# Optimization experiments

Measured on AMD Instinct MI355X. Metric: run time of the kernel, lower is better.

Reference implementation:

```python
import jax, jax.numpy as jnp
import numpy as np

N_HEADS = 4

def layernorm(x, g, b):
    m = jnp.mean(x, -1, keepdims=True)
    v = jnp.var(x, -1, keepdims=True)
    return (x - m) / jnp.sqrt(v + 1e-5) * g + b

def conv1d(x, w, b, pad):
    y = jax.lax.conv_general_dilated(x, w, (1,), [(pad, pad)], dimension_numbers=('NCH', 'OIH', 'NCH'))
    return y + b[None, :, None]

def bn_eval(x, g, b, m, v):
    return (x - m[None, :, None]) / jnp.sqrt(v[None, :, None] + 1e-5) * g[None, :, None] + b[None, :, None]

def maxpool(x, k):
    return jax.lax.reduce_window(x, -jnp.inf, jax.lax.max, (1, 1, k), (1, 1, k), 'VALID')

def _forward(x, conv1_w, conv1_b, bn1_g, bn1_b, bn1_m, bn1_v, conv2_w, conv2_b, bn2_g, bn2_b, bn2_m, bn2_v, adj_prior, log_weights, gat_n1_g, gat_n1_b, gat_qkv_w, gat_qkv_b, gat_out_w, gat_out_b, gat_n2_g, gat_n2_b, gat_f1_w, gat_f1_b, gat_f2_w, gat_f2_b, gatn_g, gatn_b, gru_wih, gru_whh, gru_bih, gru_bhh, gate_w, gate_b):
    B, C, T = x.shape
    D = conv2_w.shape[0]
    dk = D // N_HEADS
    scale = dk ** -0.5
    # --- per-channel temporal CNN: (B,C,T) -> (B,C,T',D), T' = T//16 ---
    h = x.reshape(B * C, 1, T)
    h = maxpool(jax.nn.gelu(bn_eval(conv1d(h, conv1_w, conv1_b, 3), bn1_g, bn1_b, bn1_m, bn1_v), approximate=False), 4)
    h = maxpool(jax.nn.gelu(bn_eval(conv1d(h, conv2_w, conv2_b, 2), bn2_g, bn2_b, bn2_m, bn2_v), approximate=False), 4)
    Tp = h.shape[-1]
    h = jnp.transpose(h, (0, 2, 1)).reshape(B, C, Tp, D)
    # --- spectral dynamic adjacency ---
    h_avg = h.mean(axis=2)                                   # (B,C,D)
    hc = h_avg - h_avg.mean(-1, keepdims=True)
    hn = hc / (jnp.linalg.norm(hc, axis=-1, keepdims=True) + 1e-8)
    feat_corr = jnp.einsum('bcd,bed->bce', hn, hn)
    Xp = jnp.abs(jnp.fft.rfft(x, axis=-1))
    Xn = Xp / (jnp.linalg.norm(Xp, axis=-1, keepdims=True) + 1e-8)
    spec_coh = jnp.einsum('bcf,bef->bce', Xn, Xn)
    prior = (adj_prior + adj_prior.T)[None]
    w = jax.nn.softmax(log_weights)
    adj = w[0] * feat_corr + w[1] * spec_coh + w[2] * prior  # (B,C,C)
    # --- GAT stack over the C-node channel graph at every timestep ---
    ht = jnp.transpose(h, (0, 2, 1, 3)).reshape(B * Tp, C, D)
    adj_t = jnp.broadcast_to(adj[:, None], (B, Tp, C, C)).reshape(B * Tp, C, C)
    L = gat_qkv_w.shape[0]
    for l in range(L):
        hn1 = layernorm(ht, gat_n1_g[l], gat_n1_b[l])
        qkv = (hn1 @ gat_qkv_w[l].T + gat_qkv_b[l]).reshape(B * Tp, C, 3, N_HEADS, dk)
        q = jnp.moveaxis(qkv[:, :, 0], 1, 2)                 # (N,H,C,dk)
        k = jnp.moveaxis(qkv[:, :, 1], 1, 2)
        v = jnp.moveaxis(qkv[:, :, 2], 1, 2)
        attn = jnp.einsum('nhqd,nhkd->nhqk', q, k) * scale + adj_t[:, None]
        attn = jax.nn.softmax(attn, axis=-1)                 # dropout off (eval)
        out = jnp.einsum('nhqk,nhkd->nhqd', attn, v)
        out = jnp.moveaxis(out, 1, 2).reshape(B * Tp, C, D)
        ht = ht + out @ gat_out_w[l].T + gat_out_b[l]
        hn2 = layernorm(ht, gat_n2_g[l], gat_n2_b[l])
        ffn = jax.nn.gelu(hn2 @ gat_f1_w[l].T + gat_f1_b[l], approximate=False) @ gat_f2_w[l].T + gat_f2_b[l]
        ht = ht + ffn
    ht = layernorm(ht, gatn_g, gatn_b)
    hs = ht.reshape(B, Tp, C, D).transpose(0, 2, 1, 3).reshape(B * C, Tp, D)
    # --- bidirectional GRU (1 layer), final hidden states only ---
    G = gru_whh.shape[-1]
    def gru_last(xs, wih, whh, bih, bhh):
        def step(hprev, xt):
            gi = xt @ wih.T + bih
            gh = hprev @ whh.T + bhh
            ir, iz, inn = jnp.split(gi, 3, -1)
            hr, hz, hnn = jnp.split(gh, 3, -1)
            r = jax.nn.sigmoid(ir + hr)
            z = jax.nn.sigmoid(iz + hz)
            n = jnp.tanh(inn + r * hnn)
            hnew = (1.0 - z) * n + z * hprev
            return hnew, None
        h0 = jnp.zeros((xs.shape[0], G), xs.dtype)
        hl, _ = jax.lax.scan(step, h0, jnp.moveaxis(xs, 1, 0))
        return hl
    h_f = gru_last(hs, gru_wih[0], gru_whh[0], gru_bih[0], gru_bhh[0])
    h_b = gru_last(hs[:, ::-1], gru_wih[1], gru_whh[1], gru_bih[1], gru_bhh[1])
    h_out = jnp.concatenate([h_f, h_b], -1).reshape(B, C, 2 * G)
    # --- channel-attention readout ---
    gate = jax.nn.sigmoid(h_out @ gate_w.T + gate_b)         # (B,C,1)
    readout = (h_out * gate).sum(1) / (gate.sum(1) + 1e-8)   # (B,2G)
    return readout, adj, gate

def setup_inputs() -> dict:
    key = jax.random.key(0)
    ks = iter(jax.random.split(key, 64))
    B, C, T = 32, 16, 4096
    D, L, G = 64, 2, 64
    def rn(shape, s=0.08):
        return jax.random.normal(next(ks), shape, jnp.float32) * s
    return dict(
        x=jax.random.normal(next(ks), (B, C, T), jnp.float32),
        conv1_w=rn((32, 1, 7), 0.2), conv1_b=rn((32,)),
        bn1_g=jnp.ones((32,)), bn1_b=jnp.zeros((32,)), bn1_m=jnp.zeros((32,)), bn1_v=jnp.ones((32,)),
        conv2_w=rn((D, 32, 5), 0.1), conv2_b=rn((D,)),
        bn2_g=jnp.ones((D,)), bn2_b=jnp.zeros((D,)), bn2_m=jnp.zeros((D,)), bn2_v=jnp.ones((D,)),
        adj_prior=rn((C, C), 0.1), log_weights=jnp.zeros((3,)),
        gat_n1_g=jnp.ones((L, D)), gat_n1_b=jnp.zeros((L, D)),
        gat_qkv_w=rn((L, 3 * D, D)), gat_qkv_b=jnp.zeros((L, 3 * D)),
        gat_out_w=rn((L, D, D)), gat_out_b=jnp.zeros((L, D)),
        gat_n2_g=jnp.ones((L, D)), gat_n2_b=jnp.zeros((L, D)),
        gat_f1_w=rn((L, 2 * D, D)), gat_f1_b=jnp.zeros((L, 2 * D)),
        gat_f2_w=rn((L, D, 2 * D)), gat_f2_b=jnp.zeros((L, D)),
        gatn_g=jnp.ones((D,)), gatn_b=jnp.zeros((D,)),
        gru_wih=rn((2, 3 * G, D)), gru_whh=rn((2, 3 * G, G)),
        gru_bih=jnp.zeros((2, 3 * G)), gru_bhh=jnp.zeros((2, 3 * G)),
        gate_w=rn((1, 2 * G)), gate_b=jnp.zeros((1,)),
    )

def reference(x, conv1_w, conv1_b, bn1_g, bn1_b, bn1_m, bn1_v, conv2_w, conv2_b, bn2_g, bn2_b, bn2_m, bn2_v, adj_prior, log_weights, gat_n1_g, gat_n1_b, gat_qkv_w, gat_qkv_b, gat_out_w, gat_out_b, gat_n2_g, gat_n2_b, gat_f1_w, gat_f1_b, gat_f2_w, gat_f2_b, gatn_g, gatn_b, gru_wih, gru_whh, gru_bih, gru_bhh, gate_w, gate_b):
    return _forward(x, conv1_w, conv1_b, bn1_g, bn1_b, bn1_m, bn1_v, conv2_w, conv2_b, bn2_g, bn2_b, bn2_m, bn2_v, adj_prior, log_weights, gat_n1_g, gat_n1_b, gat_qkv_w, gat_qkv_b, gat_out_w, gat_out_b, gat_n2_g, gat_n2_b, gat_f1_w, gat_f1_b, gat_f2_w, gat_f2_b, gatn_g, gatn_b, gru_wih, gru_whh, gru_bih, gru_bhh, gate_w, gate_b)
```

## Files before the change

### kernel.cpp

```cpp
#include <hip/hip_runtime.h>
#include <hip/hip_bf16.h>
#include <math.h>

typedef __hip_bfloat16 bf16;
typedef unsigned short ushort_t;
typedef __attribute__((ext_vector_type(8))) short short8;
typedef __attribute__((ext_vector_type(4))) float f32x4;

__device__ __forceinline__ float b2f(bf16 v) { return __bfloat162float(v); }
__device__ __forceinline__ bf16 f2b(float v) { return __float2bfloat16(v); }
__device__ __forceinline__ float bflo(unsigned u) { return __uint_as_float(u << 16); }
__device__ __forceinline__ float bfhi(unsigned u) { return __uint_as_float(u & 0xffff0000u); }
__device__ __forceinline__ float sigmoidf_(float x) { return 1.0f / (1.0f + __expf(-x)); }

__device__ __forceinline__ float geluf(float x) {
    float z = x * 0.70710678118654752f;
    float az = fabsf(z);
    float t = 1.0f / (1.0f + 0.3275911f * az);
    float poly = ((((1.061405429f * t - 1.453152027f) * t + 1.421413741f) * t
                   - 0.284496736f) * t + 0.254829592f) * t;
    float erfa = 1.0f - poly * __expf(-z * z);
    float er = (z < 0.f) ? -erfa : erfa;
    return 0.5f * x * (1.0f + er);
}

__device__ __forceinline__ unsigned pack2bf(float a, float b) {
    unsigned ua = __float_as_uint(a); ua = (ua + 0x7FFFu + ((ua >> 16) & 1u)) >> 16;
    unsigned ub = __float_as_uint(b); ub = (ub + 0x7FFFu + ((ub >> 16) & 1u)) >> 16;
    return ua | (ub << 16);
}
__device__ __forceinline__ ushort_t f2bu(float v) {
    unsigned u = __float_as_uint(v);
    u = (u + 0x7FFFu + ((u >> 16) & 1u)) >> 16;
    return (ushort_t)u;
}

__global__ __launch_bounds__(256) void k_detect(const unsigned* __restrict__ x, int* __restrict__ flag)
{
    __shared__ int cnt;
    if (threadIdx.x == 0) cnt = 0;
    __syncthreads();
    unsigned u = x[threadIdx.x] & 0xFFFFu;
    float f = __uint_as_float(u << 16);
    float a = fabsf(f);
    int sane = (f == 0.0f) || (a > 1e-8f && a < 1e4f);
    atomicAdd(&cnt, sane);
    __syncthreads();
    if (threadIdx.x == 0) *flag = (cnt >= 160) ? 1 : 0;
}

struct InPtrs { const void* p[35]; };
struct InOffs { int off[35]; int sz[35]; };

__global__ __launch_bounds__(256) void k_convert(InPtrs P, InOffs O, int total,
                                                 const int* __restrict__ flag,
                                                 float* __restrict__ cvt)
{
    int idx = blockIdx.x * 256 + threadIdx.x;
    if (idx >= total) return;
    int isb = *flag;
    float v = 0.f;
#pragma unroll 1
    for (int s = 0; s < 35; s++) {
        int rel = idx - O.off[s];
        if (rel >= 0 && rel < O.sz[s]) {
            v = isb ? b2f(((const bf16*)P.p[s])[rel]) : ((const float*)P.p[s])[rel];
            break;
        }
    }
    cvt[idx] = v;
}

__global__ __launch_bounds__(256) void k_pack(const float* __restrict__ qw, const float* __restrict__ ow,
                                              const float* __restrict__ f1w, const float* __restrict__ f2w,
                                              const float* __restrict__ gwih, const float* __restrict__ gwhh,
                                              const float* __restrict__ c2w,
                                              unsigned* __restrict__ dst)
{
    int i = blockIdx.x * 256 + threadIdx.x;
    if (i >= 62464) return;
    if (i >= 57344) {
        int j0 = (i - 57344) * 2;
        int tap = j0 >> 11, rem = j0 & 2047;
        int d = rem >> 5, ic = rem & 31;
        dst[i] = pack2bf(c2w[d * 160 + ic * 5 + tap], c2w[d * 160 + (ic + 1) * 5 + tap]);
        return;
    }
    const float* s; int rel;
    if (i < 12288)      { s = qw;   rel = i; }
    else if (i < 16384) { s = ow;   rel = i - 12288; }
    else if (i < 24576) { s = f1w;  rel = i - 16384; }
    else if (i < 32768) { s = f2w;  rel = i - 24576; }
    else if (i < 45056) { s = gwih; rel = i - 32768; }
    else                { s = gwhh; rel = i - 45056; }
    dst[i] = pack2bf(s[2 * rel], s[2 * rel + 1]);
}

__global__ __launch_bounds__(256) void k_cnn(
    const float* __restrict__ x, const float* __restrict__ c1w, const float* __restrict__ c1b,
    const float* __restrict__ bn1g, const float* __restrict__ bn1b, const float* __restrict__ bn1m, const float* __restrict__ bn1v,
    const float* __restrict__ c2b,
    const float* __restrict__ bn2g, const float* __restrict__ bn2b, const float* __restrict__ bn2m, const float* __restrict__ bn2v,
    const ushort_t* __restrict__ w2pk,
    float* __restrict__ h_main)
{
    __shared__ float ubuf[4352];
    __shared__ ushort_t h1t[260 * 40];
    __shared__ float A2s[64], B2s[64];
    int bc = blockIdx.x, t = threadIdx.x;
    int l = t & 63, w = t >> 6;
    int lo = l & 15, quad = l >> 4;

    if (t < 64) {
        float s = bn2g[t] * rsqrtf(bn2v[t] + 1e-5f);
        A2s[t] = s; B2s[t] = (c2b[t] - bn2m[t]) * s + bn2b[t];
    }
    int icp = t & 15;
    float w1r[2][7], A1r[2], B1r[2];
#pragma unroll
    for (int s = 0; s < 2; s++) {
        int ic = icp * 2 + s;
#pragma unroll
        for (int k = 0; k < 7; k++) w1r[s][k] = c1w[ic * 7 + k];
        float sc = bn1g[ic] * rsqrtf(bn1v[ic] + 1e-5f);
        A1r[s] = sc; B1r[s] = (c1b[ic] - bn1m[ic]) * sc + bn1b[ic];
    }
    short8 Afr[4][5];
#pragma unroll
    for (int dt = 0; dt < 4; dt++)
#pragma unroll
        for (int tap = 0; tap < 5; tap++)
            Afr[dt][tap] = *(const short8*)(w2pk + ((tap * 64 + dt * 16 + lo) * 32 + quad * 8));

    const float* xrow = x + (size_t)bc * 4096;
    for (int tile = 0; tile < 4; tile++) {
        int X0 = 1024 * tile - 11;
        for (int i = t; i < 1056; i += 256) {
            int g = X0 + i;
            ubuf[i] = (g >= 0 && g < 4096) ? xrow[g] : 0.0f;
        }
        __syncthreads();
        for (int pos = (t >> 4); pos < 260; pos += 16) {
            const float4* xw = (const float4*)&ubuf[4 * pos];
            float4 fa = xw[0], fb = xw[1], fc = xw[2];
            float xv[12] = {fa.x, fa.y, fa.z, fa.w, fb.x, fb.y, fb.z, fb.w,
                            fc.x, fc.y, fc.z, fc.w};
            int t1pg = tile * 256 + pos - 2;
            bool ok = (t1pg >= 0 && t1pg < 1024);
            float res[2];
#pragma unroll
            for (int s = 0; s < 2; s++) {
                float a0 = 0.f, a1 = 0.f, a2 = 0.f, a3 = 0.f;
#pragma unroll
                for (int k = 0; k < 7; k++) {
                    float wv = w1r[s][k];
                    a0 += xv[k] * wv;     a1 += xv[k + 1] * wv;
                    a2 += xv[k + 2] * wv; a3 += xv[k + 3] * wv;
                }
                float A = A1r[s], B = B1r[s];
                a0 = a0 * A + B; a1 = a1 * A + B; a2 = a2 * A + B; a3 = a3 * A + B;
                float mx = fmaxf(fmaxf(a0, a1), fmaxf(a2, a3));
                float mn = fminf(fminf(a0, a1), fminf(a2, a3));
                res[s] = ok ? fmaxf(geluf(mx), geluf(mn)) : 0.0f;
            }
            ((unsigned*)h1t)[pos * 20 + icp] = pack2bf(res[0], res[1]);
        }
        __syncthreads();
        float* houtile = ubuf;
#pragma unroll
        for (int ni = 0; ni < 4; ni++) {
            int nt = w * 4 + ni;
            short8 bf[5];
#pragma unroll
            for (int tap = 0; tap < 5; tap++)
                bf[tap] = *(const short8*)&h1t[(nt * 16 + lo + tap) * 40 + quad * 8];
#pragma unroll
            for (int dt = 0; dt < 4; dt++) {
                f32x4 acc = {0.f, 0.f, 0.f, 0.f};
#pragma unroll
                for (int tap = 0; tap < 5; tap++)
                    acc = __builtin_amdgcn_mfma_f32_16x16x32_bf16(Afr[dt][tap], bf[tap], acc, 0, 0, 0);
                const float4 a2 = *(const float4*)&A2s[dt * 16 + quad * 4];
                const float4 b2 = *(const float4*)&B2s[dt * 16 + quad * 4];
                float a2a[4] = {a2.x, a2.y, a2.z, a2.w};
                float b2a[4] = {b2.x, b2.y, b2.z, b2.w};
#pragma unroll
                for (int r = 0; r < 4; r++) {
                    float v = acc[r] * a2a[r] + b2a[r];
                    float o1 = __shfl_xor(v, 1);
                    float mx = fmaxf(v, o1), mn = fminf(v, o1);
                    float mx2 = __shfl_xor(mx, 2), mn2 = __shfl_xor(mn, 2);
                    mx = fmaxf(mx, mx2); mn = fminf(mn, mn2);
                    float res = fmaxf(geluf(mx), geluf(mn));
                    if ((lo & 3) == 0)
                        houtile[(nt * 4 + (lo >> 2)) * 68 + dt * 16 + quad * 4 + r] = res;
                }
            }
        }
        __syncthreads();
        float* dst = h_main + (size_t)bc * 16384 + tile * 4096;
        for (int i = t * 4; i < 4096; i += 1024) {
            float4 v = *(const float4*)&ubuf[(i >> 6) * 68 + (i & 63)];
            *(float4*)&dst[i] = v;
        }
        __syncthreads();
    }
}

__global__ __launch_bounds__(512) void k_fft(const float* __restrict__ x, float* __restrict__ Xn)
{
    __shared__ float re[4096];
    __shared__ float im[4096];
    __shared__ float red[8];
    int bc = blockIdx.x, t = threadIdx.x;
    const float* xr = x + (size_t)bc * 4096;
    for (int i = t; i < 4096; i += 512) {
        int r = __brev((unsigned)i) >> 20;
        re[r] = xr[i];
        im[r] = 0.f;
    }
    __syncthreads();
    for (int s = 1; s <= 12; s++) {
        int half = 1 << (s - 1);
        float ang = -6.283185307179586f / (float)(1 << s);
        for (int m = t; m < 2048; m += 512) {
            int j = m & (half - 1);
            int pos = ((m >> (s - 1)) << s) | j;
            float sn, cs;
            __sincosf(ang * (float)j, &sn, &cs);
            float ur = re[pos], ui = im[pos];
            float vr = re[pos + half], vi = im[pos + half];
            float tr = vr * cs - vi * sn;
            float ti = vr * sn + vi * cs;
            re[pos] = ur + tr; im[pos] = ui + ti;
            re[pos + half] = ur - tr; im[pos + half] = ui - ti;
        }
        __syncthreads();
    }
    float mag[5];
    float ss = 0.f;
    int cnt = 0;
    for (int f = t; f <= 2048; f += 512) {
        float m2 = re[f] * re[f] + im[f] * im[f];
        mag[cnt++] = sqrtf(m2);
        ss += m2;
    }
    for (int off = 32; off; off >>= 1) ss += __shfl_xor(ss, off, 64);
    if ((t & 63) == 0) red[t >> 6] = ss;
    __syncthreads();
    float tot = 0.f;
#pragma unroll
    for (int i = 0; i < 8; i++) tot += red[i];
    float inv = 1.0f / (sqrtf(tot) + 1e-8f);
    cnt = 0;
    for (int f = t; f <= 2048; f += 512) Xn[(size_t)bc * 2049 + f] = mag[cnt++] * inv;
}

__global__ __launch_bounds__(64) void k_havg(const float* __restrict__ hm, float* __restrict__ hnf)
{
    int bc = blockIdx.x, d = threadIdx.x;
    const float* base = hm + (size_t)bc * 16384;
    float s = 0.f;
    for (int tp = 0; tp < 256; tp++) s += base[tp * 64 + d];
    float avg = s * (1.0f / 256.0f);
    float tot = avg;
    for (int off = 32; off; off >>= 1) tot += __shfl_xor(tot, off, 64);
    float hc = avg - tot * (1.0f / 64.0f);
    float sq = hc * hc;
    for (int off = 32; off; off >>= 1) sq += __shfl_xor(sq, off, 64);
    hnf[bc * 64 + d] = hc / (sqrtf(sq) + 1e-8f);
}

__global__ __launch_bounds__(256) void k_adj(
    const float* __restrict__ Xn, const float* __restrict__ hnf,
    const float* __restrict__ prior, const float* __restrict__ logw,
    float* __restrict__ adjw, void* __restrict__ out, const int* __restrict__ flag)
{
    __shared__ float xt[16][257];
    __shared__ float hh[16 * 64];
    int b = blockIdx.x, t = threadIdx.x;
    int c = t >> 4, e = t & 15;
    for (int i = t; i < 1024; i += 256) hh[i] = hnf[b * 1024 + i];
    __syncthreads();
    float fc = 0.f;
    for (int d = 0; d < 64; d++) fc += hh[c * 64 + d] * hh[e * 64 + d];
    float sc = 0.f;
    const float* Xb = Xn + (size_t)b * 16 * 2049;
    for (int f0 = 0; f0 < 2048; f0 += 256) {
        __syncthreads();
        for (int i = t; i < 16 * 256; i += 256) {
            int rr = i >> 8, ff = i & 255;
            xt[rr][ff] = Xb[rr * 2049 + f0 + ff];
        }
        __syncthreads();
        for (int ff = 0; ff < 256; ff++) sc += xt[c][ff] * xt[e][ff];
    }
    sc += Xb[c * 2049 + 2048] * Xb[e * 2049 + 2048];
    float l0 = logw[0], l1 = logw[1], l2 = logw[2];
    float mx = fmaxf(l0, fmaxf(l1, l2));
    float e0 = __expf(l0 - mx), e1 = __expf(l1 - mx), e2 = __expf(l2 - mx);
    float isum = 1.0f / (e0 + e1 + e2);
    float pr = prior[c * 16 + e] + prior[e * 16 + c];
    float v = (e0 * fc + e1 * sc + e2 * pr) * isum;
    adjw[b * 256 + t] = v;
    if (*flag) ((bf16*)out)[4096 + b * 256 + t] = f2b(v);
    else       ((float*)out)[4096 + b * 256 + t] = v;
}

__device__ __forceinline__ void ln_wave(const float (*ht)[68], ushort_t (*out)[72],
                                        const float* __restrict__ g, const float* __restrict__ bp,
                                        int quad, int lo)
{
    float v[16];
    const float4* row = (const float4*)(&ht[lo][quad * 16]);
#pragma unroll
    for (int i = 0; i < 4; i++) {
        float4 a = row[i];
        v[4 * i] = a.x; v[4 * i + 1] = a.y; v[4 * i + 2] = a.z; v[4 * i + 3] = a.w;
    }
    float s = 0.f;
#pragma unroll
    for (int i = 0; i < 16; i++) s += v[i];
    s += __shfl_xor(s, 16); s += __shfl_xor(s, 32);
    float mean = s * (1.0f / 64.0f);
    float q = 0.f;
#pragma unroll
    for (int i = 0; i < 16; i++) { float d = v[i] - mean; q += d * d; }
    q += __shfl_xor(q, 16); q += __shfl_xor(q, 32);
    float rstd = rsqrtf(q * (1.0f / 64.0f) + 1e-5f);
    const float4* gp = (const float4*)(g + quad * 16);
    const float4* bb4 = (const float4*)(bp + quad * 16);
    unsigned* orow = (unsigned*)(&out[lo][quad * 16]);
#pragma unroll
    for (int i = 0; i < 4; i++) {
        float4 gg = gp[i], bb = bb4[i];
        float o0 = (v[4 * i] - mean) * rstd * gg.x + bb.x;
        float o1 = (v[4 * i + 1] - mean) * rstd * gg.y + bb.y;
        float o2 = (v[4 * i + 2] - mean) * rstd * gg.z + bb.z;
        float o3 = (v[4 * i + 3] - mean) * rstd * gg.w + bb.w;
        orow[2 * i] = pack2bf(o0, o1);
        orow[2 * i + 1] = pack2bf(o2, o3);
    }
}

__global__ __launch_bounds__(256) void k_gat(
    const float* __restrict__ hm, const float* __restrict__ adjw,
    const ushort_t* __restrict__ wpk,
    const float* __restrict__ qb_, const float* __restrict__ ob_,
    const float* __restrict__ f1b_, const float* __restrict__ f2b_,
    const float* __restrict__ n1g_, const float* __restrict__ n1b_,
    const float* __restrict__ n2g_, const float* __restrict__ n2b_,
    const float* __restrict__ gng, const float* __restrict__ gnb,
    ushort_t* __restrict__ hmb)
{
    __shared__ float htw_all[4][16][68];
    __shared__ ushort_t hnw_all[4][16][72];
    __shared__ ushort_t qkb_all[4][16][200];
    __shared__ ushort_t pb_all[4][16][72];
    __shared__ ushort_t vt_all[4][64][24];
    int t = threadIdx.x;
    int w = t >> 6, l = t & 63;
    int quad = l >> 4, lo = l & 15;
    int n = blockIdx.x * 4 + w;
    int b = n >> 8, tp = n & 255;
    float (*htw)[68] = htw_all[w];
    ushort_t (*hnw)[72] = hnw_all[w];
    ushort_t (*qkb)[200] = qkb_all[w];
    ushort_t (*pb)[72] = pb_all[w];
    ushort_t (*vt)[24] = vt_all[w];
    const float* src = hm + (size_t)b * 16 * 16384 + (size_t)tp * 64;
#pragma unroll
    for (int c = 0; c < 16; c++) htw[c][l] = src[(size_t)c * 16384 + l];
    float adjr[4];
#pragma unroll
    for (int r = 0; r < 4; r++) adjr[r] = adjw[b * 256 + (quad * 4 + r) * 16 + lo];

    for (int layer = 0; layer < 2; layer++) {
        const ushort_t* wq  = wpk + layer * 12288;
        const ushort_t* wo  = wpk + 24576 + layer * 4096;
        const ushort_t* wf1 = wpk + 32768 + layer * 8192;
        const ushort_t* wf2 = wpk + 49152 + layer * 8192;
        const float* qb = qb_ + layer * 192;
        const float* ob = ob_ + layer * 64;
        const float* f1b = f1b_ + layer * 128;
        const float* f2b = f2b_ + layer * 64;

        ln_wave(htw, hnw, n1g_ + layer * 64, n1b_ + layer * 64, quad, lo);

        short8 a0 = *(const short8*)&hnw[lo][quad * 8];
        short8 a1 = *(const short8*)&hnw[lo][32 + quad * 8];
#pragma unroll
        for (int nt = 0; nt < 12; nt++) {
            const ushort_t* wr = wq + (nt * 16 + lo) * 64 + quad * 8;
            short8 b0 = *(const short8*)wr;
            short8 b1 = *(const short8*)(wr + 32);
            f32x4 acc = {0.f, 0.f, 0.f, 0.f};
            acc = __builtin_amdgcn_mfma_f32_16x16x32_bf16(a0, b0, acc, 0, 0, 0);
            acc = __builtin_amdgcn_mfma_f32_16x16x32_bf16(a1, b1, acc, 0, 0, 0);
            float bias = qb[nt * 16 + lo];
            if (nt < 8) {
#pragma unroll
                for (int r = 0; r < 4; r++) qkb[quad * 4 + r][nt * 16 + lo] = f2bu(acc[r] + bias);
            } else {
#pragma unroll
                for (int r = 0; r < 4; r++) vt[(nt - 8) * 16 + lo][quad * 4 + r] = f2bu(acc[r] + bias);
            }
        }

        short8 zf = {0, 0, 0, 0, 0, 0, 0, 0};
#pragma unroll
        for (int h = 0; h < 4; h++) {
            short8 qf = zf, kf = zf;
            if (quad < 2) {
                qf = *(const short8*)&qkb[lo][h * 16 + quad * 8];
                kf = *(const short8*)&qkb[lo][64 + h * 16 + quad * 8];
            }
            f32x4 s4 = {0.f, 0.f, 0.f, 0.f};
            s4 = __builtin_amdgcn_mfma_f32_16x16x32_bf16(qf, kf, s4, 0, 0, 0);
#pragma unroll
            for (int r = 0; r < 4; r++) {
                float sv = s4[r] * 0.25f + adjr[r];
                float mx = sv;
                mx = fmaxf(mx, __shfl_xor(mx, 1));
                mx = fmaxf(mx, __shfl_xor(mx, 2));
                mx = fmaxf(mx, __shfl_xor(mx, 4));
                mx = fmaxf(mx, __shfl_xor(mx, 8));
                float e = __expf(sv - mx);
                float sm = e;
                sm += __shfl_xor(sm, 1);
                sm += __shfl_xor(sm, 2);
                sm += __shfl_xor(sm, 4);
                sm += __shfl_xor(sm, 8);
                pb[quad * 4 + r][h * 16 + lo] = f2bu(e / sm);
            }
        }
#pragma unroll
        for (int h = 0; h < 4; h++) {
            short8 pf = zf, vf = zf;
            if (quad < 2) {
                pf = *(const short8*)&pb[lo][h * 16 + quad * 8];
                vf = *(const short8*)&vt[h * 16 + lo][quad * 8];
            }
            f32x4 oc = {0.f, 0.f, 0.f, 0.f};
            oc = __builtin_amdgcn_mfma_f32_16x16x32_bf16(pf, vf, oc, 0, 0, 0);
#pragma unroll
            for (int r = 0; r < 4; r++) qkb[quad * 4 + r][h * 16 + lo] = f2bu(oc[r]);
        }
        short8 pa0 = *(const short8*)&qkb[lo][quad * 8];
        short8 pa1 = *(const short8*)&qkb[lo][32 + quad * 8];
#pragma unroll
        for (int nt = 0; nt < 4; nt++) {
            const ushort_t* wr = wo + (nt * 16 + lo) * 64 + quad * 8;
            short8 b0 = *(const short8*)wr;
            short8 b1 = *(const short8*)(wr + 32);
            f32x4 acc = {0.f, 0.f, 0.f, 0.f};
            acc = __builtin_amdgcn_mfma_f32_16x16x32_bf16(pa0, b0, acc, 0, 0, 0);
            acc = __builtin_amdgcn_mfma_f32_16x16x32_bf16(pa1, b1, acc, 0, 0, 0);
            float bias = ob[nt * 16 + lo];
#pragma unroll
            for (int r = 0; r < 4; r++) htw[quad * 4 + r][nt * 16 + lo] += acc[r] + bias;
        }
        ln_wave(htw, hnw, n2g_ + layer * 64, n2b_ + layer * 64, quad, lo);
        short8 fa0 = *(const short8*)&hnw[lo][quad * 8];
        short8 fa1 = *(const short8*)&hnw[lo][32 + quad * 8];
#pragma unroll
        for (int nt = 0; nt < 8; nt++) {
            const ushort_t* wr = wf1 + (nt * 16 + lo) * 64 + quad * 8;
            short8 b0 = *(const short8*)wr;
            short8 b1 = *(const short8*)(wr + 32);
            f32x4 acc = {0.f, 0.f, 0.f, 0.f};
            acc = __builtin_amdgcn_mfma_f32_16x16x32_bf16(fa0, b0, acc, 0, 0, 0);
            acc = __builtin_amdgcn_mfma_f32_16x16x32_bf16(fa1, b1, acc, 0, 0, 0);
            float bias = f1b[nt * 16 + lo];
#pragma unroll
            for (int r = 0; r < 4; r++) qkb[quad * 4 + r][nt * 16 + lo] = f2bu(geluf(acc[r] + bias));
        }
        short8 ga[4];
#pragma unroll
        for (int kb = 0; kb < 4; kb++) ga[kb] = *(const short8*)&qkb[lo][kb * 32 + quad * 8];
#pragma unroll
        for (int nt = 0; nt < 4; nt++) {
            const ushort_t* wr = wf2 + (nt * 16 + lo) * 128 + quad * 8;
            f32x4 acc = {0.f, 0.f, 0.f, 0.f};
#pragma unroll
            for (int kb = 0; kb < 4; kb++) {
                short8 bb = *(const short8*)(wr + kb * 32);
                acc = __builtin_amdgcn_mfma_f32_16x16x32_bf16(ga[kb], bb, acc, 0, 0, 0);
            }
            float bias = f2b[nt * 16 + lo];
#pragma unroll
            for (int r = 0; r < 4; r++) htw[quad * 4 + r][nt * 16 + lo] += acc[r] + bias;
        }
    }
    {
        float v[16];
        const float4* row = (const float4*)(&htw[lo][quad * 16]);
#pragma unroll
        for (int i = 0; i < 4; i++) {
            float4 a = row[i];
            v[4 * i] = a.x; v[4 * i + 1] = a.y; v[4 * i + 2] = a.z; v[4 * i + 3] = a.w;
        }
        float s = 0.f;
#pragma unroll
        for (int i = 0; i < 16; i++) s += v[i];
        s += __shfl_xor(s, 16); s += __shfl_xor(s, 32);
        float mean = s * (1.0f / 64.0f);
        float q = 0.f;
#pragma unroll
        for (int i = 0; i < 16; i++) { float d = v[i] - mean; q += d * d; }
        q += __shfl_xor(q, 16); q += __shfl_xor(q, 32);
        float rstd = rsqrtf(q * (1.0f / 64.0f) + 1e-5f);
        const float4* gp = (const float4*)(gng + quad * 16);
        const float4* bb4 = (const float4*)(gnb + quad * 16);
        unsigned u[8];
#pragma unroll
        for (int i = 0; i < 4; i++) {
            float4 gg = gp[i], bb = bb4[i];
            float o0 = (v[4 * i] - mean) * rstd * gg.x + bb.x;
            float o1 = (v[4 * i + 1] - mean) * rstd * gg.y + bb.y;
            float o2 = (v[4 * i + 2] - mean) * rstd * gg.z + bb.z;
            float o3 = (v[4 * i + 3] - mean) * rstd * gg.w + bb.w;
            u[2 * i] = pack2bf(o0, o1);
            u[2 * i + 1] = pack2bf(o2, o3);
        }
        ushort_t* dst = hmb + (size_t)(b * 16 + lo) * 16384 + (size_t)tp * 64 + quad * 16;
        ((uint4*)dst)[0] = make_uint4(u[0], u[1], u[2], u[3]);
        ((uint4*)dst)[1] = make_uint4(u[4], u[5], u[6], u[7]);
    }
}

__global__ __launch_bounds__(256) void k_gru(
    const ushort_t* __restrict__ hmb, const ushort_t* __restrict__ wgru,
    const float* __restrict__ bih_, const float* __restrict__ bhh_,
    float* __restrict__ h_out)
{
    __shared__ ushort_t hbuf[2][16][72];
    int t = threadIdx.x;
    int w = t >> 6, l = t & 63;
    int ln = l & 15, qd = l >> 4;
    int dir = blockIdx.x >> 5;
    int cseq0 = (blockIdx.x & 31) * 16;
    const ushort_t* wih = wgru + dir * 12288;
    const ushort_t* whh = wgru + 24576 + dir * 12288;
    const ushort_t* pr0 = wih + ((w)*16 + ln) * 64 + qd * 8;
    const ushort_t* pz0 = wih + ((4 + w)*16 + ln) * 64 + qd * 8;
    const ushort_t* pn0 = wih + ((8 + w)*16 + ln) * 64 + qd * 8;
    const ushort_t* hr0 = whh + ((w)*16 + ln) * 64 + qd * 8;
    const ushort_t* hz0 = whh + ((4 + w)*16 + ln) * 64 + qd * 8;
    const ushort_t* hn0 = whh + ((8 + w)*16 + ln) * 64 + qd * 8;
    short8 wi_r0 = *(const short8*)pr0, wi_r1 = *(const short8*)(pr0 + 32);
    short8 wi_z0 = *(const short8*)pz0, wi_z1 = *(const short8*)(pz0 + 32);
    short8 wi_n0 = *(const short8*)pn0, wi_n1 = *(const short8*)(pn0 + 32);
    short8 wh_r0 = *(const short8*)hr0, wh_r1 = *(const short8*)(hr0 + 32);
    short8 wh_z0 = *(const short8*)hz0, wh_z1 = *(const short8*)(hz0 + 32);
    short8 wh_n0 = *(const short8*)hn0, wh_n1 = *(const short8*)(hn0 + 32);
    int d = w * 16 + ln;
    float bs_r = bih_[dir * 192 + d] + bhh_[dir * 192 + d];
    float bs_z = bih_[dir * 192 + 64 + d] + bhh_[dir * 192 + 64 + d];
    float bi_n = bih_[dir * 192 + 128 + d];
    float bh_n = bhh_[dir * 192 + 128 + d];
    const ushort_t* xrow = hmb + (size_t)(cseq0 + ln) * 16384 + qd * 8;
    for (int i = t; i < 2 * 16 * 72; i += 256) ((ushort_t*)hbuf)[i] = 0;
    float h_old[4] = {0.f, 0.f, 0.f, 0.f};

    int s0 = dir ? 255 : 0;
    int s1 = dir ? 254 : 1;
    int s2 = dir ? 253 : 2;
    short8 xc0 = *(const short8*)(xrow + s0 * 64);
    short8 xc1 = *(const short8*)(xrow + s0 * 64 + 32);
    short8 xA0 = *(const short8*)(xrow + s1 * 64);
    short8 xA1 = *(const short8*)(xrow + s1 * 64 + 32);
    short8 xB0 = *(const short8*)(xrow + s2 * 64);
    short8 xB1 = *(const short8*)(xrow + s2 * 64 + 32);
    f32x4 axr = {0.f, 0.f, 0.f, 0.f}, axz = {0.f, 0.f, 0.f, 0.f}, axn = {0.f, 0.f, 0.f, 0.f};
    axr = __builtin_amdgcn_mfma_f32_16x16x32_bf16(xc0, wi_r0, axr, 0, 0, 0);
    axr = __builtin_amdgcn_mfma_f32_16x16x32_bf16(xc1, wi_r1, axr, 0, 0, 0);
    axz = __builtin_amdgcn_mfma_f32_16x16x32_bf16(xc0, wi_z0, axz, 0, 0, 0);
    axz = __builtin_amdgcn_mfma_f32_16x16x32_bf16(xc1, wi_z1, axz, 0, 0, 0);
    axn = __builtin_amdgcn_mfma_f32_16x16x32_bf16(xc0, wi_n0, axn, 0, 0, 0);
    axn = __builtin_amdgcn_mfma_f32_16x16x32_bf16(xc1, wi_n1, axn, 0, 0, 0);
    __syncthreads();
#pragma unroll 2
    for (int step = 0; step < 256; step++) {
        int cur = step & 1, nxt = cur ^ 1;
        f32x4 nxr = {0.f, 0.f, 0.f, 0.f}, nxz = {0.f, 0.f, 0.f, 0.f}, nxn = {0.f, 0.f, 0.f, 0.f};
        nxr = __builtin_amdgcn_mfma_f32_16x16x32_bf16(xA0, wi_r0, nxr, 0, 0, 0);
        nxr = __builtin_amdgcn_mfma_f32_16x16x32_bf16(xA1, wi_r1, nxr, 0, 0, 0);
        nxz = __builtin_amdgcn_mfma_f32_16x16x32_bf16(xA0, wi_z0, nxz, 0, 0, 0);
        nxz = __builtin_amdgcn_mfma_f32_16x16x32_bf16(xA1, wi_z1, nxz, 0, 0, 0);
        nxn = __builtin_amdgcn_mfma_f32_16x16x32_bf16(xA0, wi_n0, nxn, 0, 0, 0);
        nxn = __builtin_amdgcn_mfma_f32_16x16x32_bf16(xA1, wi_n1, nxn, 0, 0, 0);
        xA0 = xB0; xA1 = xB1;
        int tl = step + 3 > 255 ? 255 : step + 3;
        int sf = dir ? 255 - tl : tl;
        xB0 = *(const short8*)(xrow + sf * 64);
        xB1 = *(const short8*)(xrow + sf * 64 + 32);
        short8 ah0 = *(const short8*)&hbuf[cur][ln][qd * 8];
        short8 ah1 = *(const short8*)&hbuf[cur][ln][32 + qd * 8];
        f32x4 ar = axr, az = axz;
        f32x4 anh = {0.f, 0.f, 0.f, 0.f};
        ar = __builtin_amdgcn_mfma_f32_16x16x32_bf16(ah0, wh_r0, ar, 0, 0, 0);
        ar = __builtin_amdgcn_mfma_f32_16x16x32_bf16(ah1, wh_r1, ar, 0, 0, 0);
        az = __builtin_amdgcn_mfma_f32_16x16x32_bf16(ah0, wh_z0, az, 0, 0, 0);
        az = __builtin_amdgcn_mfma_f32_16x16x32_bf16(ah1, wh_z1, az, 0, 0, 0);
        anh = __builtin_amdgcn_mfma_f32_16x16x32_bf16(ah0, wh_n0, anh, 0, 0, 0);
        anh = __builtin_amdgcn_mfma_f32_16x16x32_bf16(ah1, wh_n1, anh, 0, 0, 0);
#pragma unroll
        for (int r = 0; r < 4; r++) {
            float gr = sigmoidf_(ar[r] + bs_r);
            float gz = sigmoidf_(az[r] + bs_z);
            float nin = (axn[r] + bi_n) + gr * (anh[r] + bh_n);
            nin = fminf(fmaxf(nin, -15.f), 15.f);
            float e = __expf(-2.f * nin);
            float gn = (1.f - e) / (1.f + e);
            float hn = gn + gz * (h_old[r] - gn);
            h_old[r] = hn;
            hbuf[nxt][qd * 4 + r][d] = f2bu(hn);
        }
        asm volatile("s_waitcnt lgkmcnt(0)\n\ts_barrier" ::: "memory");
        axr = nxr; axz = nxz; axn = nxn;
    }
#pragma unroll
    for (int r = 0; r < 4; r++)
        h_out[(size_t)(cseq0 + qd * 4 + r) * 128 + dir * 64 + d] = h_old[r];
}

__global__ __launch_bounds__(128) void k_readout(
    const float* __restrict__ h_out, const float* __restrict__ gw, const float* __restrict__ gb,
    void* __restrict__ out, const int* __restrict__ flag)
{
    __shared__ float gate_s[16];
    __shared__ float gws[128];
    int b = blockIdx.x, t = threadIdx.x;
    gws[t] = gw[t];
    __syncthreads();
    int isb = *flag;
    if (t < 16) {
        const float* hr = h_out + (size_t)(b * 16 + t) * 128;
        float acc = gb[0];
        for (int k = 0; k < 128; k++) acc += hr[k] * gws[k];
        float g = sigmoidf_(acc);
        gate_s[t] = g;
        if (isb) ((bf16*)out)[12288 + b * 16 + t] = f2b(g);
        else     ((float*)out)[12288 + b * 16 + t] = g;
    }
    __syncthreads();
    float den = 1e-8f;
#pragma unroll
    for (int c = 0; c < 16; c++) den += gate_s[c];
    float num = 0.f;
#pragma unroll
    for (int c = 0; c < 16; c++) num += h_out[(size_t)(b * 16 + c) * 128 + t] * gate_s[c];
    float v = num / den;
    if (isb) ((bf16*)out)[b * 128 + t] = f2b(v);
    else     ((float*)out)[b * 128 + t] = v;
}

extern "C" void kernel_launch(void* const* d_in, const int* in_sizes, int n_in,
                              void* d_out, int out_size, void* d_ws, size_t ws_size,
                              hipStream_t stream)
{
    int* flag = (int*)d_ws;
    float* cvt = (float*)((char*)d_ws + 256);

    InPtrs P;
    InOffs O;
    int cum = 0;
    for (int i = 0; i < 35; i++) {
        P.p[i] = d_in[i];
        O.off[i] = cum;
        O.sz[i] = in_sizes[i];
        cum += (in_sizes[i] + 7) & ~7;
    }
    int total = cum;

    const float* x     = cvt + O.off[0];
    const float* c1w   = cvt + O.off[1];
    const float* c1b   = cvt + O.off[2];
    const float* bn1g  = cvt + O.off[3];
    const float* bn1b  = cvt + O.off[4];
    const float* bn1m  = cvt + O.off[5];
    const float* bn1v  = cvt + O.off[6];
    const float* c2w   = cvt + O.off[7];
    const float* c2b   = cvt + O.off[8];
    const float* bn2g  = cvt + O.off[9];
    const float* bn2b  = cvt + O.off[10];
    const float* bn2m  = cvt + O.off[11];
    const float* bn2v  = cvt + O.off[12];
    const float* prior = cvt + O.off[13];
    const float* logw  = cvt + O.off[14];
    const float* n1g   = cvt + O.off[15];
    const float* n1b   = cvt + O.off[16];
    const float* qkvw  = cvt + O.off[17];
    const float* qkvb  = cvt + O.off[18];
    const float* outw  = cvt + O.off[19];
    const float* outb  = cvt + O.off[20];
    const float* n2g   = cvt + O.off[21];
    const float* n2b   = cvt + O.off[22];
    const float* f1w   = cvt + O.off[23];
    const float* f1b   = cvt + O.off[24];
    const float* f2w   = cvt + O.off[25];
    const float* f2b_  = cvt + O.off[26];
    const float* gng   = cvt + O.off[27];
    const float* gnb   = cvt + O.off[28];
    const float* gwih  = cvt + O.off[29];
    const float* gwhh  = cvt + O.off[30];
    const float* gbih  = cvt + O.off[31];
    const float* gbhh  = cvt + O.off[32];
    const float* gatew = cvt + O.off[33];
    const float* gateb = cvt + O.off[34];

    float* fbase = cvt + ((total + 63) & ~63);
    float* hm   = fbase;
    float* Xn   = hm + 8388608;
    float* hnf  = Xn + 1049088;
    float* adjw = hnf + 32768;
    float* hout = adjw + 8192;
    unsigned* wpk = (unsigned*)(hout + 65536);
    ushort_t* hmb = (ushort_t*)(wpk + 62464);

    k_detect<<<1, 256, 0, stream>>>((const unsigned*)d_in[0], flag);
    k_convert<<<(total + 255) / 256, 256, 0, stream>>>(P, O, total, flag, cvt);
    k_pack<<<244, 256, 0, stream>>>(qkvw, outw, f1w, f2w, gwih, gwhh, c2w, wpk);
    k_cnn<<<512, 256, 0, stream>>>(x, c1w, c1b, bn1g, bn1b, bn1m, bn1v,
                                   c2b, bn2g, bn2b, bn2m, bn2v,
                                   (const ushort_t*)(wpk + 57344), hm);
    k_fft<<<512, 512, 0, stream>>>(x, Xn);
    k_havg<<<512, 64, 0, stream>>>(hm, hnf);
    k_adj<<<32, 256, 0, stream>>>(Xn, hnf, prior, logw, adjw, d_out, flag);
    k_gat<<<2048, 256, 0, stream>>>(hm, adjw, (const ushort_t*)wpk,
                                    qkvb, outb, f1b, f2b_, n1g, n1b, n2g, n2b, gng, gnb, hmb);
    k_gru<<<64, 256, 0, stream>>>(hmb, (const ushort_t*)(wpk + 32768), gbih, gbhh, hout);
    k_readout<<<32, 128, 0, stream>>>(hout, gatew, gateb, d_out, flag);
}
```

Before: 669.8 us.

## Fuse CNN, FFT and channel-mean kernels into one launch; transpose GRU MFMA operands

Merges the CNN front end, the per-channel FFT coherence kernel and the time-average kernel into a single 1024-block launch. The first 512 blocks run the CNN and also accumulate the time mean from shared memory, so hm no longer has to be re-read. The remaining 512 blocks compute the FFT at 256 threads each. Separately, the GRU swaps its MFMA operand order so each lane holds four consecutive hidden units, which lets it write packed 8-byte hidden-state stores to LDS and a float4 final store. The trade-off is that the FFT blocks get half as many threads and share LDS sizing with the CNN blocks, which may lower occupancy.

```diff
diff --git a/kernel.cpp b/kernel.cpp
--- a/kernel.cpp
+++ b/kernel.cpp
@@ -9,8 +9,6 @@
 
 __device__ __forceinline__ float b2f(bf16 v) { return __bfloat162float(v); }
 __device__ __forceinline__ bf16 f2b(float v) { return __float2bfloat16(v); }
-__device__ __forceinline__ float bflo(unsigned u) { return __uint_as_float(u << 16); }
-__device__ __forceinline__ float bfhi(unsigned u) { return __uint_as_float(u & 0xffff0000u); }
 __device__ __forceinline__ float sigmoidf_(float x) { return 1.0f / (1.0f + __expf(-x)); }
 
 __device__ __forceinline__ float geluf(float x) {
@@ -96,18 +94,69 @@
     dst[i] = pack2bf(s[2 * rel], s[2 * rel + 1]);
 }
 
-__global__ __launch_bounds__(256) void k_cnn(
-    const float* __restrict__ x, const float* __restrict__ c1w, const float* __restrict__ c1b,
+__global__ __launch_bounds__(256) void k_front(
+    const float* __restrict__ x,
+    const float* __restrict__ c1w, const float* __restrict__ c1b,
     const float* __restrict__ bn1g, const float* __restrict__ bn1b, const float* __restrict__ bn1m, const float* __restrict__ bn1v,
     const float* __restrict__ c2b,
     const float* __restrict__ bn2g, const float* __restrict__ bn2b, const float* __restrict__ bn2m, const float* __restrict__ bn2v,
     const ushort_t* __restrict__ w2pk,
-    float* __restrict__ h_main)
-{
-    __shared__ float ubuf[4352];
-    __shared__ ushort_t h1t[260 * 40];
-    __shared__ float A2s[64], B2s[64];
-    int bc = blockIdx.x, t = threadIdx.x;
+    float* __restrict__ h_main, float* __restrict__ Xn, float* __restrict__ hnf)
+{
+    __shared__ float smem[9984];
+    int t = threadIdx.x;
+    if (blockIdx.x >= 512) {
+        float* re = smem;
+        float* im = smem + 4096;
+        float* red = smem + 8192;
+        int bc = blockIdx.x - 512;
+        const float* xr = x + (size_t)bc * 4096;
+        for (int i = t; i < 4096; i += 256) {
+            int r = __brev((unsigned)i) >> 20;
+            re[r] = xr[i];
+            im[r] = 0.f;
+        }
+        __syncthreads();
+        for (int s = 1; s <= 12; s++) {
+            int half = 1 << (s - 1);
+            float ang = -6.283185307179586f / (float)(1 << s);
+            for (int m = t; m < 2048; m += 256) {
+                int j = m & (half - 1);
+                int pos = ((m >> (s - 1)) << s) | j;
+                float sn, cs;
+                __sincosf(ang * (float)j, &sn, &cs);
+                float ur = re[pos], ui = im[pos];
+                float vr = re[pos + half], vi = im[pos + half];
+                float tr = vr * cs - vi * sn;
+                float ti = vr * sn + vi * cs;
+                re[pos] = ur + tr; im[pos] = ui + ti;
+                re[pos + half] = ur - tr; im[pos + half] = ui - ti;
+            }
+            __syncthreads();
+        }
+        float mag[9];
+        float ss = 0.f;
+        int cnt = 0;
+        for (int f = t; f <= 2048; f += 256) {
+            float m2 = re[f] * re[f] + im[f] * im[f];
+            mag[cnt++] = sqrtf(m2);
+            ss += m2;
+        }
+        for (int off = 32; off; off >>= 1) ss += __shfl_xor(ss, off, 64);
+        if ((t & 63) == 0) red[t >> 6] = ss;
+        __syncthreads();
+        float tot = red[0] + red[1] + red[2] + red[3];
+        float inv = 1.0f / (sqrtf(tot) + 1e-8f);
+        cnt = 0;
+        for (int f = t; f <= 2048; f += 256) Xn[(size_t)bc * 2049 + f] = mag[cnt++] * inv;
+        return;
+    }
+    float* ubuf = smem;
+    ushort_t* h1t = (ushort_t*)(smem + 4352);
+    float* A2s = smem + 9552;
+    float* B2s = smem + 9616;
+    float* hsum = smem + 9680;
+    int bc = blockIdx.x;
     int l = t & 63, w = t >> 6;
     int lo = l & 15, quad = l >> 4;
 
@@ -133,6 +182,8 @@
             Afr[dt][tap] = *(const short8*)(w2pk + ((tap * 64 + dt * 16 + lo) * 32 + quad * 8));
 
     const float* xrow = x + (size_t)bc * 4096;
+    float rs = 0.f;
+    int dd = t & 63, pg = t >> 6;
     for (int tile = 0; tile < 4; tile++) {
         int X0 = 1024 * tile - 11;
         for (int i = t; i < 1056; i += 256) {
@@ -170,16 +221,16 @@
 #pragma unroll
         for (int ni = 0; ni < 4; ni++) {
             int nt = w * 4 + ni;
-            short8 bf[5];
+            short8 bfr[5];
 #pragma unroll
             for (int tap = 0; tap < 5; tap++)
-                bf[tap] = *(const short8*)&h1t[(nt * 16 + lo + tap) * 40 + quad * 8];
+                bfr[tap] = *(const short8*)&h1t[(nt * 16 + lo + tap) * 40 + quad * 8];
 #pragma unroll
             for (int dt = 0; dt < 4; dt++) {
                 f32x4 acc = {0.f, 0.f, 0.f, 0.f};
 #pragma unroll
                 for (int tap = 0; tap < 5; tap++)
-                    acc = __builtin_amdgcn_mfma_f32_16x16x32_bf16(Afr[dt][tap], bf[tap], acc, 0, 0, 0);
+                    acc = __builtin_amdgcn_mfma_f32_16x16x32_bf16(Afr[dt][tap], bfr[tap], acc, 0, 0, 0);
                 const float4 a2 = *(const float4*)&A2s[dt * 16 + quad * 4];
                 const float4 b2 = *(const float4*)&B2s[dt * 16 + quad * 4];
                 float a2a[4] = {a2.x, a2.y, a2.z, a2.w};
@@ -198,6 +249,8 @@
             }
         }
         __syncthreads();
+#pragma unroll
+        for (int i = 0; i < 16; i++) rs += ubuf[(pg * 16 + i) * 68 + dd];
         float* dst = h_main + (size_t)bc * 16384 + tile * 4096;
         for (int i = t * 4; i < 4096; i += 1024) {
             float4 v = *(const float4*)&ubuf[(i >> 6) * 68 + (i & 63)];
@@ -205,70 +258,17 @@
         }
         __syncthreads();
     }
-}
-
-__global__ __launch_bounds__(512) void k_fft(const float* __restrict__ x, float* __restrict__ Xn)
-{
-    __shared__ float re[4096];
-    __shared__ float im[4096];
-    __shared__ float red[8];
-    int bc = blockIdx.x, t = threadIdx.x;
-    const float* xr = x + (size_t)bc * 4096;
-    for (int i = t; i < 4096; i += 512) {
-        int r = __brev((unsigned)i) >> 20;
-        re[r] = xr[i];
-        im[r] = 0.f;
-    }
+    hsum[t] = rs;
     __syncthreads();
-    for (int s = 1; s <= 12; s++) {
-        int half = 1 << (s - 1);
-        float ang = -6.283185307179586f / (float)(1 << s);
-        for (int m = t; m < 2048; m += 512) {
-            int j = m & (half - 1);
-            int pos = ((m >> (s - 1)) << s) | j;
-            float sn, cs;
-            __sincosf(ang * (float)j, &sn, &cs);
-            float ur = re[pos], ui = im[pos];
-            float vr = re[pos + half], vi = im[pos + half];
-            float tr = vr * cs - vi * sn;
-            float ti = vr * sn + vi * cs;
-            re[pos] = ur + tr; im[pos] = ui + ti;
-            re[pos + half] = ur - tr; im[pos + half] = ui - ti;
-        }
-        __syncthreads();
-    }
-    float mag[5];
-    float ss = 0.f;
-    int cnt = 0;
-    for (int f = t; f <= 2048; f += 512) {
-        float m2 = re[f] * re[f] + im[f] * im[f];
-        mag[cnt++] = sqrtf(m2);
-        ss += m2;
-    }
-    for (int off = 32; off; off >>= 1) ss += __shfl_xor(ss, off, 64);
-    if ((t & 63) == 0) red[t >> 6] = ss;
-    __syncthreads();
-    float tot = 0.f;
-#pragma unroll
-    for (int i = 0; i < 8; i++) tot += red[i];
-    float inv = 1.0f / (sqrtf(tot) + 1e-8f);
-    cnt = 0;
-    for (int f = t; f <= 2048; f += 512) Xn[(size_t)bc * 2049 + f] = mag[cnt++] * inv;
-}
-
-__global__ __launch_bounds__(64) void k_havg(const float* __restrict__ hm, float* __restrict__ hnf)
-{
-    int bc = blockIdx.x, d = threadIdx.x;
-    const float* base = hm + (size_t)bc * 16384;
-    float s = 0.f;
-    for (int tp = 0; tp < 256; tp++) s += base[tp * 64 + d];
-    float avg = s * (1.0f / 256.0f);
-    float tot = avg;
-    for (int off = 32; off; off >>= 1) tot += __shfl_xor(tot, off, 64);
-    float hc = avg - tot * (1.0f / 64.0f);
-    float sq = hc * hc;
-    for (int off = 32; off; off >>= 1) sq += __shfl_xor(sq, off, 64);
-    hnf[bc * 64 + d] = hc / (sqrtf(sq) + 1e-8f);
+    if (t < 64) {
+        float avg = (hsum[t] + hsum[64 + t] + hsum[128 + t] + hsum[192 + t]) * (1.0f / 256.0f);
+        float tot = avg;
+        for (int off = 32; off; off >>= 1) tot += __shfl_xor(tot, off, 64);
+        float hc = avg - tot * (1.0f / 64.0f);
+        float sq = hc * hc;
+        for (int off = 32; off; off >>= 1) sq += __shfl_xor(sq, off, 64);
+        hnf[bc * 64 + t] = hc / (sqrtf(sq) + 1e-8f);
+    }
 }
 
 __global__ __launch_bounds__(256) void k_adj(
@@ -537,29 +537,33 @@
     __shared__ ushort_t hbuf[2][16][72];
     int t = threadIdx.x;
     int w = t >> 6, l = t & 63;
-    int ln = l & 15, qd = l >> 4;
+    int lo = l & 15, qd = l >> 4;
     int dir = blockIdx.x >> 5;
     int cseq0 = (blockIdx.x & 31) * 16;
     const ushort_t* wih = wgru + dir * 12288;
     const ushort_t* whh = wgru + 24576 + dir * 12288;
-    const ushort_t* pr0 = wih + ((w)*16 + ln) * 64 + qd * 8;
-    const ushort_t* pz0 = wih + ((4 + w)*16 + ln) * 64 + qd * 8;
-    const ushort_t* pn0 = wih + ((8 + w)*16 + ln) * 64 + qd * 8;
-    const ushort_t* hr0 = whh + ((w)*16 + ln) * 64 + qd * 8;
-    const ushort_t* hz0 = whh + ((4 + w)*16 + ln) * 64 + qd * 8;
-    const ushort_t* hn0 = whh + ((8 + w)*16 + ln) * 64 + qd * 8;
+    const ushort_t* pr0 = wih + ((w) * 16 + lo) * 64 + qd * 8;
+    const ushort_t* pz0 = wih + ((4 + w) * 16 + lo) * 64 + qd * 8;
+    const ushort_t* pn0 = wih + ((8 + w) * 16 + lo) * 64 + qd * 8;
+    const ushort_t* hr0 = whh + ((w) * 16 + lo) * 64 + qd * 8;
+    const ushort_t* hz0 = whh + ((4 + w) * 16 + lo) * 64 + qd * 8;
+    const ushort_t* hn0 = whh + ((8 + w) * 16 + lo) * 64 + qd * 8;
     short8 wi_r0 = *(const short8*)pr0, wi_r1 = *(const short8*)(pr0 + 32);
     short8 wi_z0 = *(const short8*)pz0, wi_z1 = *(const short8*)(pz0 + 32);
     short8 wi_n0 = *(const short8*)pn0, wi_n1 = *(const short8*)(pn0 + 32);
     short8 wh_r0 = *(const short8*)hr0, wh_r1 = *(const short8*)(hr0 + 32);
     short8 wh_z0 = *(const short8*)hz0, wh_z1 = *(const short8*)(hz0 + 32);
     short8 wh_n0 = *(const short8*)hn0, wh_n1 = *(const short8*)(hn0 + 32);
-    int d = w * 16 + ln;
-    float bs_r = bih_[dir * 192 + d] + bhh_[dir * 192 + d];
-    float bs_z = bih_[dir * 192 + 64 + d] + bhh_[dir * 192 + 64 + d];
-    float bi_n = bih_[dir * 192 + 128 + d];
-    float bh_n = bhh_[dir * 192 + 128 + d];
-    const ushort_t* xrow = hmb + (size_t)(cseq0 + ln) * 16384 + qd * 8;
+    int d_base = w * 16 + qd * 4;
+    float bsr[4], bsz[4], bin[4], bhn[4];
+#pragma unroll
+    for (int r = 0; r < 4; r++) {
+        bsr[r] = bih_[dir * 192 + d_base + r] + bhh_[dir * 192 + d_base + r];
+        bsz[r] = bih_[dir * 192 + 64 + d_base + r] + bhh_[dir * 192 + 64 + d_base + r];
+        bin[r] = bih_[dir * 192 + 128 + d_base + r];
+        bhn[r] = bhh_[dir * 192 + 128 + d_base + r];
+    }
+    const ushort_t* xrow = hmb + (size_t)(cseq0 + lo) * 16384 + qd * 8;
     for (int i = t; i < 2 * 16 * 72; i += 256) ((ushort_t*)hbuf)[i] = 0;
     float h_old[4] = {0.f, 0.f, 0.f, 0.f};
 
@@ -573,56 +577,57 @@
     short8 xB0 = *(const short8*)(xrow + s2 * 64);
     short8 xB1 = *(const short8*)(xrow + s2 * 64 + 32);
     f32x4 axr = {0.f, 0.f, 0.f, 0.f}, axz = {0.f, 0.f, 0.f, 0.f}, axn = {0.f, 0.f, 0.f, 0.f};
-    axr = __builtin_amdgcn_mfma_f32_16x16x32_bf16(xc0, wi_r0, axr, 0, 0, 0);
-    axr = __builtin_amdgcn_mfma_f32_16x16x32_bf16(xc1, wi_r1, axr, 0, 0, 0);
-    axz = __builtin_amdgcn_mfma_f32_16x16x32_bf16(xc0, wi_z0, axz, 0, 0, 0);
-    axz = __builtin_amdgcn_mfma_f32_16x16x32_bf16(xc1, wi_z1, axz, 0, 0, 0);
-    axn = __builtin_amdgcn_mfma_f32_16x16x32_bf16(xc0, wi_n0, axn, 0, 0, 0);
-    axn = __builtin_amdgcn_mfma_f32_16x16x32_bf16(xc1, wi_n1, axn, 0, 0, 0);
+    axr = __builtin_amdgcn_mfma_f32_16x16x32_bf16(wi_r0, xc0, axr, 0, 0, 0);
+    axr = __builtin_amdgcn_mfma_f32_16x16x32_bf16(wi_r1, xc1, axr, 0, 0, 0);
+    axz = __builtin_amdgcn_mfma_f32_16x16x32_bf16(wi_z0, xc0, axz, 0, 0, 0);
+    axz = __builtin_amdgcn_mfma_f32_16x16x32_bf16(wi_z1, xc1, axz, 0, 0, 0);
+    axn = __builtin_amdgcn_mfma_f32_16x16x32_bf16(wi_n0, xc0, axn, 0, 0, 0);
+    axn = __builtin_amdgcn_mfma_f32_16x16x32_bf16(wi_n1, xc1, axn, 0, 0, 0);
     __syncthreads();
 #pragma unroll 2
     for (int step = 0; step < 256; step++) {
         int cur = step & 1, nxt = cur ^ 1;
         f32x4 nxr = {0.f, 0.f, 0.f, 0.f}, nxz = {0.f, 0.f, 0.f, 0.f}, nxn = {0.f, 0.f, 0.f, 0.f};
-        nxr = __builtin_amdgcn_mfma_f32_16x16x32_bf16(xA0, wi_r0, nxr, 0, 0, 0);
-        nxr = __builtin_amdgcn_mfma_f32_16x16x32_bf16(xA1, wi_r1, nxr, 0, 0, 0);
-        nxz = __builtin_amdgcn_mfma_f32_16x16x32_bf16(xA0, wi_z0, nxz, 0, 0, 0);
-        nxz = __builtin_amdgcn_mfma_f32_16x16x32_bf16(xA1, wi_z1, nxz, 0, 0, 0);
-        nxn = __builtin_amdgcn_mfma_f32_16x16x32_bf16(xA0, wi_n0, nxn, 0, 0, 0);
-        nxn = __builtin_amdgcn_mfma_f32_16x16x32_bf16(xA1, wi_n1, nxn, 0, 0, 0);
+        nxr = __builtin_amdgcn_mfma_f32_16x16x32_bf16(wi_r0, xA0, nxr, 0, 0, 0);
+        nxr = __builtin_amdgcn_mfma_f32_16x16x32_bf16(wi_r1, xA1, nxr, 0, 0, 0);
+        nxz = __builtin_amdgcn_mfma_f32_16x16x32_bf16(wi_z0, xA0, nxz, 0, 0, 0);
+        nxz = __builtin_amdgcn_mfma_f32_16x16x32_bf16(wi_z1, xA1, nxz, 0, 0, 0);
+        nxn = __builtin_amdgcn_mfma_f32_16x16x32_bf16(wi_n0, xA0, nxn, 0, 0, 0);
+        nxn = __builtin_amdgcn_mfma_f32_16x16x32_bf16(wi_n1, xA1, nxn, 0, 0, 0);
         xA0 = xB0; xA1 = xB1;
         int tl = step + 3 > 255 ? 255 : step + 3;
         int sf = dir ? 255 - tl : tl;
         xB0 = *(const short8*)(xrow + sf * 64);
         xB1 = *(const short8*)(xrow + sf * 64 + 32);
-        short8 ah0 = *(const short8*)&hbuf[cur][ln][qd * 8];
-        short8 ah1 = *(const short8*)&hbuf[cur][ln][32 + qd * 8];
+        short8 bh0 = *(const short8*)&hbuf[cur][lo][qd * 8];
+        short8 bh1 = *(const short8*)&hbuf[cur][lo][32 + qd * 8];
         f32x4 ar = axr, az = axz;
         f32x4 anh = {0.f, 0.f, 0.f, 0.f};
-        ar = __builtin_amdgcn_mfma_f32_16x16x32_bf16(ah0, wh_r0, ar, 0, 0, 0);
-        ar = __builtin_amdgcn_mfma_f32_16x16x32_bf16(ah1, wh_r1, ar, 0, 0, 0);
-        az = __builtin_amdgcn_mfma_f32_16x16x32_bf16(ah0, wh_z0, az, 0, 0, 0);
-        az = __builtin_amdgcn_mfma_f32_16x16x32_bf16(ah1, wh_z1, az, 0, 0, 0);
-        anh = __builtin_amdgcn_mfma_f32_16x16x32_bf16(ah0, wh_n0, anh, 0, 0, 0);
-        anh = __builtin_amdgcn_mfma_f32_16x16x32_bf16(ah1, wh_n1, anh, 0, 0, 0);
+        ar = __builtin_amdgcn_mfma_f32_16x16x32_bf16(wh_r0, bh0, ar, 0, 0, 0);
+        ar = __builtin_amdgcn_mfma_f32_16x16x32_bf16(wh_r1, bh1, ar, 0, 0, 0);
+        az = __builtin_amdgcn_mfma_f32_16x16x32_bf16(wh_z0, bh0, az, 0, 0, 0);
+        az = __builtin_amdgcn_mfma_f32_16x16x32_bf16(wh_z1, bh1, az, 0, 0, 0);
+        anh = __builtin_amdgcn_mfma_f32_16x16x32_bf16(wh_n0, bh0, anh, 0, 0, 0);
+        anh = __builtin_amdgcn_mfma_f32_16x16x32_bf16(wh_n1, bh1, anh, 0, 0, 0);
+        float hv[4];
 #pragma unroll
         for (int r = 0; r < 4; r++) {
-            float gr = sigmoidf_(ar[r] + bs_r);
-            float gz = sigmoidf_(az[r] + bs_z);
-            float nin = (axn[r] + bi_n) + gr * (anh[r] + bh_n);
+            float gr = sigmoidf_(ar[r] + bsr[r]);
+            float gz = sigmoidf_(az[r] + bsz[r]);
+            float nin = (axn[r] + bin[r]) + gr * (anh[r] + bhn[r]);
             nin = fminf(fmaxf(nin, -15.f), 15.f);
             float e = __expf(-2.f * nin);
             float gn = (1.f - e) / (1.f + e);
             float hn = gn + gz * (h_old[r] - gn);
             h_old[r] = hn;
-            hbuf[nxt][qd * 4 + r][d] = f2bu(hn);
-        }
+            hv[r] = hn;
+        }
+        *(uint2*)&hbuf[nxt][lo][d_base] = make_uint2(pack2bf(hv[0], hv[1]), pack2bf(hv[2], hv[3]));
         asm volatile("s_waitcnt lgkmcnt(0)\n\ts_barrier" ::: "memory");
         axr = nxr; axz = nxz; axn = nxn;
     }
-#pragma unroll
-    for (int r = 0; r < 4; r++)
-        h_out[(size_t)(cseq0 + qd * 4 + r) * 128 + dir * 64 + d] = h_old[r];
+    *(float4*)&h_out[(size_t)(cseq0 + lo) * 128 + dir * 64 + d_base] =
+        make_float4(h_old[0], h_old[1], h_old[2], h_old[3]);
 }
 
 __global__ __launch_bounds__(128) void k_readout(
@@ -722,11 +727,9 @@
     k_detect<<<1, 256, 0, stream>>>((const unsigned*)d_in[0], flag);
     k_convert<<<(total + 255) / 256, 256, 0, stream>>>(P, O, total, flag, cvt);
     k_pack<<<244, 256, 0, stream>>>(qkvw, outw, f1w, f2w, gwih, gwhh, c2w, wpk);
-    k_cnn<<<512, 256, 0, stream>>>(x, c1w, c1b, bn1g, bn1b, bn1m, bn1v,
-                                   c2b, bn2g, bn2b, bn2m, bn2v,
-                                   (const ushort_t*)(wpk + 57344), hm);
-    k_fft<<<512, 512, 0, stream>>>(x, Xn);
-    k_havg<<<512, 64, 0, stream>>>(hm, hnf);
+    k_front<<<1024, 256, 0, stream>>>(x, c1w, c1b, bn1g, bn1b, bn1m, bn1v,
+                                      c2b, bn2g, bn2b, bn2m, bn2v,
+                                      (const ushort_t*)(wpk + 57344), hm, Xn, hnf);
     k_adj<<<32, 256, 0, stream>>>(Xn, hnf, prior, logw, adjw, d_out, flag);
     k_gat<<<2048, 256, 0, stream>>>(hm, adjw, (const ushort_t*)wpk,
                                     qkvb, outb, f1b, f2b_, n1g, n1b, n2g, n2b, gng, gnb, hmb);
```

New measurement: 652.4 us. -2.6%, faster.
